# Kernel tuning notes

Hardware: AMD Instinct MI355X
Metric: run time of the kernel (lower is better)

The kernel has to match this reference:

```python
import jax, jax.numpy as jnp
import numpy as np

ALPHA = 2.0      # spikingjelly surrogate.ATan default alpha
TAU_LIF = 2.0    # LIFNode tau
V_TH = 1.0       # spike threshold (v_reset = 0.0, hard reset)


@jax.custom_vjp
def spike_fn(x):
    # Heaviside forward (spikingjelly: x >= 0 -> 1)
    return (x >= 0.0).astype(x.dtype)

def _spike_fwd(x):
    return spike_fn(x), x

def _spike_bwd(x, g):
    # ATan surrogate gradient: alpha/2 / (1 + (pi/2 * alpha * x)^2)
    return (g * (ALPHA / 2.0) / (1.0 + (jnp.pi / 2.0 * ALPHA * x) ** 2),)

spike_fn.defvjp(_spike_fwd, _spike_bwd)


def setup_inputs() -> dict:
    key = jax.random.key(0)
    ks = jax.random.split(key, 5)
    B, T, I, H, O = 256, 1000, 700, 64, 20
    x = jax.random.normal(ks[0], (B, T, I), dtype=jnp.float32)
    W_h = jax.random.normal(ks[1], (H, I), dtype=jnp.float32) / np.sqrt(I).astype(np.float32)
    b_h = jnp.zeros((H,), dtype=jnp.float32)
    W_r = jax.random.normal(ks[2], (O, H), dtype=jnp.float32) / np.sqrt(H).astype(np.float32)
    b_r = jnp.zeros((O,), dtype=jnp.float32)
    tau_m = jax.random.uniform(ks[3], (O,), dtype=jnp.float32, minval=0.0, maxval=4.0)
    return {"x": x, "W_h": W_h, "b_h": b_h, "W_r": W_r, "b_r": b_r, "tau_m": tau_m}


def reference(x, W_h, b_h, W_r, b_r, tau_m):
    B, T, I = x.shape
    H = W_h.shape[0]
    O = W_r.shape[0]
    # One big GEMM for all hidden input currents: [T, B, H]
    currents = jnp.einsum('bti,hi->tbh', x, W_h) + b_h
    beta = jax.nn.sigmoid(tau_m)  # readout leak [O]
    # original accumulates softmax only for t > 10
    mask = (jnp.arange(T) > 10).astype(x.dtype)

    def step(carry, inp):
        v, v_ro, acc = carry
        cur, m = inp
        # LIF charge (decay_input=True, v_reset=0): v += (cur - v)/tau
        v = v + (cur - v) / TAU_LIF
        s = spike_fn(v - V_TH)
        # hard reset to v_reset = 0
        v = v * (1.0 - s)
        # readout leaky integrator
        ro_in = s @ W_r.T + b_r                      # [B, O]
        v_ro = v_ro * beta + (1.0 - beta) * ro_in
        acc = acc + m * jax.nn.softmax(v_ro, axis=-1)
        return (v, v_ro, acc), None

    init = (jnp.zeros((B, H), x.dtype),
            jnp.zeros((B, O), x.dtype),
            jnp.zeros((B, O), x.dtype))
    (_, _, acc), _ = jax.lax.scan(step, init, (currents, mask))
    return acc
```

## Files before the change

### kernel.cpp

```cpp
#include <hip/hip_runtime.h>


typedef float  f32x4  __attribute__((ext_vector_type(4)));
typedef short  short8 __attribute__((ext_vector_type(8)));
typedef unsigned long long ull;

#define B_   256
#define T_   1000
#define K_   700
#define H_   64
#define O_   20
#define NKT  11
#define NCH  200
#define TCH  5
#define TCL  100
#define NCL  10
#define BIL  40

#define OFF_WFRAG  ((size_t)0)
#define OFF_CUR    ((size_t)262144)
#define OFF_MASK   ((size_t)65798144)

__global__ void wprep(const float* __restrict__ Wh, unsigned short* __restrict__ wfrag) {
    int e = blockIdx.x * 256 + threadIdx.x;
    int kt   = e >> 9;
    int rem  = e & 511;
    int nf   = rem >> 7;
    int kf   = (rem >> 6) & 1;
    int lane = rem & 63;
    int h     = nf * 16 + (lane & 15);
    int kbase = kt * 64 + kf * 32 + ((lane >> 4) & 3) * 8;
    int slot  = (nf * 2 + kf) * 64 + lane;
    unsigned short* dh = wfrag + (size_t)kt * 8192 + slot * 8;
    unsigned short* dl = dh + 4096;
#pragma unroll
    for (int j = 0; j < 8; ++j) {
        int k = kbase + j;
        float v = (k < K_) ? Wh[(size_t)h * K_ + k] : 0.0f;
        unsigned u  = __builtin_bit_cast(unsigned, v);
        float    fh = __builtin_bit_cast(float, u & 0xffff0000u);
        float    r  = v - fh;
        dh[j] = (unsigned short)(u >> 16);
        dl[j] = (unsigned short)(__builtin_bit_cast(unsigned, r) >> 16);
    }
}

__device__ __forceinline__ void glds16(const void* src, void* lds) {
    __builtin_amdgcn_global_load_lds(
        (const __attribute__((address_space(1))) void*)src,
        (__attribute__((address_space(3))) void*)lds, 16, 0, 0);
}

__device__ __forceinline__ void splitpair(f32x4 p0, f32x4 p1, short8& hi, short8& lo) {
#pragma unroll
    for (int j = 0; j < 4; ++j) {
        {
            unsigned u  = __builtin_bit_cast(unsigned, p0[j]);
            float    fh = __builtin_bit_cast(float, u & 0xffff0000u);
            float    r  = p0[j] - fh;
            hi[j] = (short)(u >> 16);
            lo[j] = (short)(__builtin_bit_cast(unsigned, r) >> 16);
        }
        {
            unsigned u  = __builtin_bit_cast(unsigned, p1[j]);
            float    fh = __builtin_bit_cast(float, u & 0xffff0000u);
            float    r  = p1[j] - fh;
            hi[j + 4] = (short)(u >> 16);
            lo[j + 4] = (short)(__builtin_bit_cast(unsigned, r) >> 16);
        }
    }
}

__device__ __forceinline__ void stage_x64(const float* __restrict__ x, size_t row0,
                                          int kt, int tid, float* sbuf) {
#pragma unroll
    for (int j = 0; j < 4; ++j) {
        int id = j * 256 + tid;
        int s  = id >> 9;
        int r  = (id >> 3) & 63;
        int pc = id & 7;
        int c  = pc ^ (r & 7);
        int kbyte = kt * 256 + s * 128 + (c << 4);
        if (kbyte + 16 > K_ * 4) kbyte = 0;
        const char* src = (const char*)(x + (row0 + r) * (size_t)K_) + kbyte;
        float* dst = sbuf + (size_t)(id & ~63) * 4;
        glds16(src, dst);
    }
}

__device__ __forceinline__ void stage_w64(const unsigned short* __restrict__ wfrag,
                                          int kt, int tid, unsigned short* sbuf) {
#pragma unroll
    for (int j = 0; j < 4; ++j) {
        int id = j * 256 + tid;
        const unsigned short* src = wfrag + (size_t)kt * 8192 + id * 8;
        unsigned short* dst = sbuf + (size_t)(id & ~63) * 8;
        glds16(src, dst);
    }
}

__device__ __forceinline__ void compute64(const float* sbx_, const unsigned short* sbw_,
                                          int lane, int wid, f32x4 (&acc)[4]) {
    const char*   xb = (const char*)sbx_;
    const short8* wb = (const short8*)sbw_;
    int rloc = wid * 16 + (lane & 15);
    int g2   = ((lane >> 4) & 3) * 2;
#pragma unroll
    for (int kf = 0; kf < 2; ++kf) {
        const char* base = xb + kf * 8192 + rloc * 128;
        int c0 = g2 ^ (rloc & 7);
        int c1 = (g2 + 1) ^ (rloc & 7);
        f32x4 p0 = *(const f32x4*)(base + c0 * 16);
        f32x4 p1 = *(const f32x4*)(base + c1 * 16);
        short8 ah, al;
        splitpair(p0, p1, ah, al);
#pragma unroll
        for (int n = 0; n < 4; ++n) {
            short8 bhf = wb[(n * 2 + kf) * 64 + lane];
            short8 blf = wb[(n * 2 + kf) * 64 + lane + 512];
            acc[n] = __builtin_amdgcn_mfma_f32_16x16x32_bf16(ah, bhf, acc[n], 0, 0, 0);
            acc[n] = __builtin_amdgcn_mfma_f32_16x16x32_bf16(al, bhf, acc[n], 0, 0, 0);
            acc[n] = __builtin_amdgcn_mfma_f32_16x16x32_bf16(ah, blf, acc[n], 0, 0, 0);
        }
    }
}

__global__ __launch_bounds__(256, 2) void gemm_cur(const float* __restrict__ x,
                                                   const unsigned short* __restrict__ wfrag,
                                                   const float* __restrict__ b_h,
                                                   float* __restrict__ cur) {
    __shared__ float          sbx[2][4096];
    __shared__ unsigned short sbw[2][8192];
    int tid  = threadIdx.x;
    int lane = tid & 63;
    int wid  = tid >> 6;
    size_t row0 = (size_t)blockIdx.x * 64;

    float bh4[4];
#pragma unroll
    for (int n = 0; n < 4; ++n) bh4[n] = b_h[n * 16 + (lane & 15)];

    f32x4 acc[4];
#pragma unroll
    for (int n = 0; n < 4; ++n) acc[n] = (f32x4){0.f, 0.f, 0.f, 0.f};

    stage_x64(x, row0, 0, tid, sbx[0]);  stage_w64(wfrag, 0, tid, sbw[0]);
    stage_x64(x, row0, 1, tid, sbx[1]);  stage_w64(wfrag, 1, tid, sbw[1]);

#define GSTEP(T, N)                                                          \
    {                                                                        \
        asm volatile("s_waitcnt vmcnt(" #N ")" ::: "memory");                \
        __builtin_amdgcn_s_barrier();                                        \
        compute64(sbx[(T) & 1], sbw[(T) & 1], lane, wid, acc);               \
        asm volatile("s_waitcnt lgkmcnt(0)" ::: "memory");                   \
        __builtin_amdgcn_s_barrier();                                        \
        if ((T) + 2 < NKT) {                                                 \
            stage_x64(x, row0, (T) + 2, tid, sbx[(T) & 1]);                  \
            stage_w64(wfrag, (T) + 2, tid, sbw[(T) & 1]);                    \
        }                                                                    \
    }
    GSTEP(0, 8)   GSTEP(1, 8)   GSTEP(2, 8)   GSTEP(3, 8)   GSTEP(4, 8)
    GSTEP(5, 8)   GSTEP(6, 8)   GSTEP(7, 8)   GSTEP(8, 8)   GSTEP(9, 8)
    GSTEP(10, 0)
#undef GSTEP

    f32x4* cur4 = (f32x4*)cur;
    size_t r4 = row0 + wid * 16 + ((lane >> 4) & 3) * 4;
#pragma unroll
    for (int n = 0; n < 4; ++n) {
        f32x4 q;
#pragma unroll
        for (int j = 0; j < 4; ++j) q[j] = acc[n][j] + bh4[n];
        cur4[(r4 >> 2) * 64 + n * 16 + (lane & 15)] = q;
    }
}

__global__ __launch_bounds__(64) void lif(const float* __restrict__ cur, ull* __restrict__ masks) {
    int b = blockIdx.x & 255;
    int c = blockIdx.x >> 8;
    int h = threadIdx.x;
    int t0 = c * TCL;
    int ts = (c == 0) ? 0 : (t0 - BIL);
    const f32x4* p = (const f32x4*)cur + (((size_t)b * T_ + ts) >> 2) * 64 + h;
    float v = 0.0f;
    int ngb = (t0 - ts) >> 2;
    for (int g = 0; g < ngb; ++g) {
        f32x4 q = p[g * 64];
#pragma unroll
        for (int j = 0; j < 4; ++j) {
            v = (v + q[j]) * 0.5f;
            v = (v >= 1.0f) ? 0.0f : v;
        }
    }
    p += (size_t)ngb * 64;
    ull* mp = masks + (size_t)b * T_ + t0;
#pragma unroll 2
    for (int g = 0; g < TCL / 4; ++g) {
        f32x4 q = p[g * 64];
#pragma unroll
        for (int j = 0; j < 4; ++j) {
            v = (v + q[j]) * 0.5f;
            bool s = (v >= 1.0f);
            ull m = __ballot(s);
            if (h == 0) mp[g * 4 + j] = m;
            v = s ? 0.0f : v;
        }
    }
}

__global__ __launch_bounds__(512) void readout(const ull* __restrict__ masks,
                                               const float* __restrict__ Wr,
                                               const float* __restrict__ br,
                                               const float* __restrict__ tau,
                                               float* __restrict__ out) {
    __shared__ __align__(16) float wt[64][20];
    __shared__ ull  smask[T_];
    __shared__ __align__(16) float E[NCH][20];
    __shared__ __align__(16) float Sv[NCH][20];
    __shared__ __align__(16) float pacc[NCH][20];
    __shared__ __align__(16) float sScale[20], sBase[20], sBeta[20];
    __shared__ float Pg[8][20], Sst[8][20], part[8][20];

    int tid = threadIdx.x;
    int b   = blockIdx.x;
    for (int i = tid; i < 1280; i += 512) wt[i & 63][i >> 6] = Wr[(size_t)(i >> 6) * 64 + (i & 63)];
    for (int i = tid; i < T_; i += 512) smask[i] = masks[(size_t)b * T_ + i];
    if (tid < 20) {
        float beta = 1.0f / (1.0f + __expf(-tau[tid]));
        sBeta[tid]  = beta;
        sScale[tid] = 1.0f - beta;
        sBase[tid]  = br[tid];
    }
    __syncthreads();

    for (int it = tid; it < NCH * 5; it += 512) {
        int o4 = it % 5;
        int c  = it / 5;
        f32x4 beta4  = *(const f32x4*)&sBeta[o4 * 4];
        f32x4 scale4 = *(const f32x4*)&sScale[o4 * 4];
        f32x4 base4  = *(const f32x4*)&sBase[o4 * 4];
        f32x4 v = {0.f, 0.f, 0.f, 0.f};
        const ull* mp = smask + c * TCH;
#pragma unroll
        for (int j = 0; j < TCH; ++j) {
            ull m = mp[j];
            f32x4 a = {0.f, 0.f, 0.f, 0.f};
            while (m) {
                int h = __builtin_ctzll(m);
                m &= (m - 1);
                a += *(const f32x4*)&wt[h][o4 * 4];
            }
            f32x4 q;
#pragma unroll
            for (int jj = 0; jj < 4; ++jj) q[jj] = scale4[jj] * (base4[jj] + a[jj]);
            v = beta4 * v + q;
        }
        *(f32x4*)&E[c][o4 * 4] = v;
    }
    __syncthreads();

    if (tid < 160) {
        int o = tid >> 3, g = tid & 7;
        float beta = sBeta[o];
        float b2 = beta * beta;
        float bp = b2 * b2 * beta;
        float P = 0.0f;
        for (int c = g * 25; c < g * 25 + 25; ++c) P = bp * P + E[c][o];
        Pg[g][o] = P;
    }
    __syncthreads();

    if (tid < 20) {
        int o = tid;
        float beta = sBeta[o];
        float b2 = beta * beta;
        float bp = b2 * b2 * beta;
        float bp25 = 1.0f;
#pragma unroll
        for (int i = 0; i < 25; ++i) bp25 *= bp;
        float s = 0.0f;
        for (int g = 0; g < 8; ++g) { Sst[g][o] = s; s = bp25 * s + Pg[g][o]; }
    }
    __syncthreads();

    if (tid < 160) {
        int o = tid >> 3, g = tid & 7;
        float beta = sBeta[o];
        float b2 = beta * beta;
        float bp = b2 * b2 * beta;
        float s = Sst[g][o];
        for (int c = g * 25; c < g * 25 + 25; ++c) { Sv[c][o] = s; s = bp * s + E[c][o]; }
    }
    __syncthreads();

    if (tid < NCH) {
        int c = tid;
        float beta[20], v[20], acc[20];
#pragma unroll
        for (int o = 0; o < 20; ++o) {
            beta[o] = sBeta[o];
            v[o]   = Sv[c][o];
            acc[o] = 0.0f;
        }
        int t0 = c * TCH;
        const ull* mp = smask + t0;
#pragma unroll
        for (int j = 0; j < TCH; ++j) {
            int t = t0 + j;
            ull m = mp[j];
            f32x4 a[5];
#pragma unroll
            for (int i = 0; i < 5; ++i) a[i] = (f32x4){0.f, 0.f, 0.f, 0.f};
            while (m) {
                int h = __builtin_ctzll(m);
                m &= (m - 1);
                const f32x4* w4 = (const f32x4*)&wt[h][0];
#pragma unroll
                for (int i = 0; i < 5; ++i) a[i] += w4[i];
            }
#pragma unroll
            for (int o = 0; o < 20; ++o) {
                float q = sScale[o] * (sBase[o] + a[o >> 2][o & 3]);
                v[o] = beta[o] * v[o] + q;
            }
            if (t >= 11) {
                float mx = v[0];
#pragma unroll
                for (int o = 1; o < 20; ++o) mx = fmaxf(mx, v[o]);
                float e[20], ssum = 0.0f;
#pragma unroll
                for (int o = 0; o < 20; ++o) { e[o] = __expf(v[o] - mx); ssum += e[o]; }
                float inv = 1.0f / ssum;
#pragma unroll
                for (int o = 0; o < 20; ++o) acc[o] += e[o] * inv;
            }
        }
#pragma unroll
        for (int o = 0; o < 20; ++o) pacc[c][o] = acc[o];
    }
    __syncthreads();

    if (tid < 160) {
        int o = tid >> 3, g = tid & 7;
        float s = 0.0f;
        for (int c = g * 25; c < g * 25 + 25; ++c) s += pacc[c][o];
        part[g][o] = s;
    }
    __syncthreads();
    if (tid < 20) {
        float s = 0.0f;
#pragma unroll
        for (int g = 0; g < 8; ++g) s += part[g][tid];
        out[(size_t)b * 20 + tid] = s;
    }
}

extern "C" void kernel_launch(void* const* d_in, const int* in_sizes, int n_in,
                              void* d_out, int out_size, void* d_ws, size_t ws_size,
                              hipStream_t stream) {
    const float* x   = (const float*)d_in[0];
    const float* W_h = (const float*)d_in[1];
    const float* b_h = (const float*)d_in[2];
    const float* W_r = (const float*)d_in[3];
    const float* b_r = (const float*)d_in[4];
    const float* tau = (const float*)d_in[5];

    char* ws = (char*)d_ws;
    unsigned short* wfrag = (unsigned short*)(ws + OFF_WFRAG);
    float* cur  = (float*)(ws + OFF_CUR);
    ull*   msk  = (ull*)(ws + OFF_MASK);
    float* out  = (float*)d_out;

    wprep<<<22, 256, 0, stream>>>(W_h, wfrag);
    gemm_cur<<<4000, 256, 0, stream>>>(x, wfrag, b_h, cur);
    lif<<<NCL * 256, 64, 0, stream>>>(cur, msk);
    readout<<<256, 512, 0, stream>>>(msk, W_r, b_r, tau, out);
}
```

Baseline: 222.1 us.

## Fuse GEMM, LIF scan and readout into one per-batch kernel

Replaces the separate current-GEMM, LIF and readout kernels with a single kernel that runs one 512-thread block per batch element. Each block streams its own x rows in 128-timestep tiles, writes the input currents for a tile into shared memory, runs the LIF recurrence there to build spike masks, then runs the existing readout in reused shared memory. This avoids the global round trip of the large current tensor and two kernel launches. In exchange, the grid shrinks to 256 large blocks with heavy LDS use, likely one block per CU. The serial LIF phase between tiles also stalls the GEMM load pipeline, which may hurt memory-bandwidth utilisation.

```diff
diff --git a/kernel.cpp b/kernel.cpp
--- a/kernel.cpp
+++ b/kernel.cpp
@@ -11,15 +11,11 @@
 #define H_   64
 #define O_   20
 #define NKT  11
+#define NMT  8
 #define NCH  200
 #define TCH  5
-#define TCL  100
-#define NCL  10
-#define BIL  40
 
 #define OFF_WFRAG  ((size_t)0)
-#define OFF_CUR    ((size_t)262144)
-#define OFF_MASK   ((size_t)65798144)
 
 __global__ void wprep(const float* __restrict__ Wh, unsigned short* __restrict__ wfrag) {
     int e = blockIdx.x * 256 + threadIdx.x;
@@ -71,43 +67,45 @@
     }
 }
 
-__device__ __forceinline__ void stage_x64(const float* __restrict__ x, size_t row0,
-                                          int kt, int tid, float* sbuf) {
+__device__ __forceinline__ void stage_x(const float* __restrict__ x, size_t brow0,
+                                        int mt, int kt, int tid, float* sbuf) {
 #pragma unroll
     for (int j = 0; j < 4; ++j) {
-        int id = j * 256 + tid;
-        int s  = id >> 9;
-        int r  = (id >> 3) & 63;
+        int id = j * 512 + tid;
+        int s2 = id >> 10;
+        int r  = (id >> 3) & 127;
         int pc = id & 7;
         int c  = pc ^ (r & 7);
-        int kbyte = kt * 256 + s * 128 + (c << 4);
+        int trow = mt * 128 + r;
+        if (trow >= T_) trow = 0;
+        int kbyte = kt * 256 + s2 * 128 + (c << 4);
         if (kbyte + 16 > K_ * 4) kbyte = 0;
-        const char* src = (const char*)(x + (row0 + r) * (size_t)K_) + kbyte;
+        const char* src = (const char*)(x + (brow0 + trow) * (size_t)K_) + kbyte;
         float* dst = sbuf + (size_t)(id & ~63) * 4;
         glds16(src, dst);
     }
 }
 
-__device__ __forceinline__ void stage_w64(const unsigned short* __restrict__ wfrag,
-                                          int kt, int tid, unsigned short* sbuf) {
-#pragma unroll
-    for (int j = 0; j < 4; ++j) {
-        int id = j * 256 + tid;
+__device__ __forceinline__ void stage_w(const unsigned short* __restrict__ wfrag,
+                                        int kt, int tid, unsigned short* sbuf) {
+#pragma unroll
+    for (int j = 0; j < 2; ++j) {
+        int id = j * 512 + tid;
         const unsigned short* src = wfrag + (size_t)kt * 8192 + id * 8;
         unsigned short* dst = sbuf + (size_t)(id & ~63) * 8;
         glds16(src, dst);
     }
 }
 
-__device__ __forceinline__ void compute64(const float* sbx_, const unsigned short* sbw_,
-                                          int lane, int wid, f32x4 (&acc)[4]) {
+__device__ __forceinline__ void compute128(const float* sbx_, const unsigned short* sbw_,
+                                           int lane, int wid, f32x4 (&acc)[4]) {
     const char*   xb = (const char*)sbx_;
     const short8* wb = (const short8*)sbw_;
     int rloc = wid * 16 + (lane & 15);
     int g2   = ((lane >> 4) & 3) * 2;
 #pragma unroll
     for (int kf = 0; kf < 2; ++kf) {
-        const char* base = xb + kf * 8192 + rloc * 128;
+        const char* base = xb + kf * 16384 + rloc * 128;
         int c0 = g2 ^ (rloc & 7);
         int c1 = (g2 + 1) ^ (rloc & 7);
         f32x4 p0 = *(const f32x4*)(base + c0 * 16);
@@ -125,16 +123,27 @@
     }
 }
 
-__global__ __launch_bounds__(256, 2) void gemm_cur(const float* __restrict__ x,
-                                                   const unsigned short* __restrict__ wfrag,
-                                                   const float* __restrict__ b_h,
-                                                   float* __restrict__ cur) {
-    __shared__ float          sbx[2][4096];
-    __shared__ unsigned short sbw[2][8192];
+__global__ __launch_bounds__(512, 2) void fused(const float* __restrict__ x,
+                                                const unsigned short* __restrict__ wfrag,
+                                                const float* __restrict__ b_h,
+                                                const float* __restrict__ Wr,
+                                                const float* __restrict__ br,
+                                                const float* __restrict__ tau,
+                                                float* __restrict__ out) {
+    __shared__ __align__(16) char  pool[98304];
+    __shared__ __align__(16) float curT[128 * 64];
+    __shared__ ull smaskL[T_];
+
     int tid  = threadIdx.x;
     int lane = tid & 63;
     int wid  = tid >> 6;
-    size_t row0 = (size_t)blockIdx.x * 64;
+    int b    = blockIdx.x;
+    size_t brow0 = (size_t)b * T_;
+
+    float*          sbx0 = (float*)pool;
+    float*          sbx1 = (float*)(pool + 32768);
+    unsigned short* sbw0 = (unsigned short*)(pool + 65536);
+    unsigned short* sbw1 = (unsigned short*)(pool + 81920);
 
     float bh4[4];
 #pragma unroll
@@ -143,88 +152,71 @@
     f32x4 acc[4];
 #pragma unroll
     for (int n = 0; n < 4; ++n) acc[n] = (f32x4){0.f, 0.f, 0.f, 0.f};
-
-    stage_x64(x, row0, 0, tid, sbx[0]);  stage_w64(wfrag, 0, tid, sbw[0]);
-    stage_x64(x, row0, 1, tid, sbx[1]);  stage_w64(wfrag, 1, tid, sbw[1]);
-
-#define GSTEP(T, N)                                                          \
-    {                                                                        \
-        asm volatile("s_waitcnt vmcnt(" #N ")" ::: "memory");                \
-        __builtin_amdgcn_s_barrier();                                        \
-        compute64(sbx[(T) & 1], sbw[(T) & 1], lane, wid, acc);               \
-        asm volatile("s_waitcnt lgkmcnt(0)" ::: "memory");                   \
-        __builtin_amdgcn_s_barrier();                                        \
-        if ((T) + 2 < NKT) {                                                 \
-            stage_x64(x, row0, (T) + 2, tid, sbx[(T) & 1]);                  \
-            stage_w64(wfrag, (T) + 2, tid, sbw[(T) & 1]);                    \
-        }                                                                    \
-    }
-    GSTEP(0, 8)   GSTEP(1, 8)   GSTEP(2, 8)   GSTEP(3, 8)   GSTEP(4, 8)
-    GSTEP(5, 8)   GSTEP(6, 8)   GSTEP(7, 8)   GSTEP(8, 8)   GSTEP(9, 8)
-    GSTEP(10, 0)
-#undef GSTEP
-
-    f32x4* cur4 = (f32x4*)cur;
-    size_t r4 = row0 + wid * 16 + ((lane >> 4) & 3) * 4;
-#pragma unroll
-    for (int n = 0; n < 4; ++n) {
-        f32x4 q;
-#pragma unroll
-        for (int j = 0; j < 4; ++j) q[j] = acc[n][j] + bh4[n];
-        cur4[(r4 >> 2) * 64 + n * 16 + (lane & 15)] = q;
-    }
-}
-
-__global__ __launch_bounds__(64) void lif(const float* __restrict__ cur, ull* __restrict__ masks) {
-    int b = blockIdx.x & 255;
-    int c = blockIdx.x >> 8;
-    int h = threadIdx.x;
-    int t0 = c * TCL;
-    int ts = (c == 0) ? 0 : (t0 - BIL);
-    const f32x4* p = (const f32x4*)cur + (((size_t)b * T_ + ts) >> 2) * 64 + h;
     float v = 0.0f;
-    int ngb = (t0 - ts) >> 2;
-    for (int g = 0; g < ngb; ++g) {
-        f32x4 q = p[g * 64];
-#pragma unroll
-        for (int j = 0; j < 4; ++j) {
-            v = (v + q[j]) * 0.5f;
-            v = (v >= 1.0f) ? 0.0f : v;
-        }
-    }
-    p += (size_t)ngb * 64;
-    ull* mp = masks + (size_t)b * T_ + t0;
-#pragma unroll 2
-    for (int g = 0; g < TCL / 4; ++g) {
-        f32x4 q = p[g * 64];
-#pragma unroll
-        for (int j = 0; j < 4; ++j) {
-            v = (v + q[j]) * 0.5f;
-            bool s = (v >= 1.0f);
-            ull m = __ballot(s);
-            if (h == 0) mp[g * 4 + j] = m;
-            v = s ? 0.0f : v;
-        }
-    }
-}
-
-__global__ __launch_bounds__(512) void readout(const ull* __restrict__ masks,
-                                               const float* __restrict__ Wr,
-                                               const float* __restrict__ br,
-                                               const float* __restrict__ tau,
-                                               float* __restrict__ out) {
-    __shared__ __align__(16) float wt[64][20];
-    __shared__ ull  smask[T_];
-    __shared__ __align__(16) float E[NCH][20];
-    __shared__ __align__(16) float Sv[NCH][20];
-    __shared__ __align__(16) float pacc[NCH][20];
-    __shared__ __align__(16) float sScale[20], sBase[20], sBeta[20];
-    __shared__ float Pg[8][20], Sst[8][20], part[8][20];
-
-    int tid = threadIdx.x;
-    int b   = blockIdx.x;
-    for (int i = tid; i < 1280; i += 512) wt[i & 63][i >> 6] = Wr[(size_t)(i >> 6) * 64 + (i & 63)];
-    for (int i = tid; i < T_; i += 512) smask[i] = masks[(size_t)b * T_ + i];
+
+    stage_x(x, brow0, 0, 0, tid, sbx0);  stage_w(wfrag, 0, tid, sbw0);
+    stage_x(x, brow0, 0, 1, tid, sbx1);  stage_w(wfrag, 1, tid, sbw1);
+
+    int p = 0;
+    for (int mt = 0; mt < NMT; ++mt) {
+#pragma unroll
+        for (int kt = 0; kt <= 10; ++kt) {
+            float*          xb = p ? sbx1 : sbx0;
+            unsigned short* wb = p ? sbw1 : sbw0;
+            if (kt == 10 && mt == NMT - 1) {
+                asm volatile("s_waitcnt vmcnt(0)" ::: "memory");
+            } else {
+                asm volatile("s_waitcnt vmcnt(6)" ::: "memory");
+            }
+            __builtin_amdgcn_s_barrier();
+            compute128(xb, wb, lane, wid, acc);
+            if (kt == 10) {
+#pragma unroll
+                for (int n = 0; n < 4; ++n) {
+#pragma unroll
+                    for (int j = 0; j < 4; ++j) {
+                        int tloc = wid * 16 + ((lane >> 4) & 3) * 4 + j;
+                        curT[tloc * 64 + n * 16 + (lane & 15)] = acc[n][j] + bh4[n];
+                    }
+                    acc[n] = (f32x4){0.f, 0.f, 0.f, 0.f};
+                }
+            }
+            asm volatile("s_waitcnt lgkmcnt(0)" ::: "memory");
+            __builtin_amdgcn_s_barrier();
+            int smt = mt, skt = kt + 2;
+            if (skt >= NKT) { smt += 1; skt -= NKT; }
+            if (smt < NMT) {
+                stage_x(x, brow0, smt, skt, tid, xb);
+                stage_w(wfrag, skt, tid, wb);
+            }
+            p ^= 1;
+            if (kt == 10) {
+                int tcnt = T_ - mt * 128; if (tcnt > 128) tcnt = 128;
+                for (int j = 0; j < tcnt; ++j) {
+                    float c = curT[j * 64 + lane];
+                    v = (v + c) * 0.5f;
+                    bool sp = (v >= 1.0f);
+                    ull m = __ballot(sp);
+                    if (wid == (j >> 4) && lane == 0) smaskL[mt * 128 + j] = m;
+                    v = sp ? 0.0f : v;
+                }
+            }
+        }
+    }
+    __syncthreads();
+
+    float* wt     = (float*)pool;
+    float (*E)[20]    = (float(*)[20])(pool + 5120);
+    float (*Sv)[20]   = (float(*)[20])(pool + 21120);
+    float (*pacc)[20] = (float(*)[20])(pool + 37120);
+    float* sScale = (float*)(pool + 53120);
+    float* sBase  = (float*)(pool + 53216);
+    float* sBeta  = (float*)(pool + 53312);
+    float (*Pg)[20]   = (float(*)[20])(pool + 53408);
+    float (*Sst)[20]  = (float(*)[20])(pool + 54048);
+    float (*part)[20] = (float(*)[20])(pool + 54688);
+
+    for (int i = tid; i < 1280; i += 512) wt[(i & 63) * 20 + (i >> 6)] = Wr[(size_t)(i >> 6) * 64 + (i & 63)];
     if (tid < 20) {
         float beta = 1.0f / (1.0f + __expf(-tau[tid]));
         sBeta[tid]  = beta;
@@ -239,8 +231,8 @@
         f32x4 beta4  = *(const f32x4*)&sBeta[o4 * 4];
         f32x4 scale4 = *(const f32x4*)&sScale[o4 * 4];
         f32x4 base4  = *(const f32x4*)&sBase[o4 * 4];
-        f32x4 v = {0.f, 0.f, 0.f, 0.f};
-        const ull* mp = smask + c * TCH;
+        f32x4 vv = {0.f, 0.f, 0.f, 0.f};
+        const ull* mp = smaskL + c * TCH;
 #pragma unroll
         for (int j = 0; j < TCH; ++j) {
             ull m = mp[j];
@@ -248,14 +240,14 @@
             while (m) {
                 int h = __builtin_ctzll(m);
                 m &= (m - 1);
-                a += *(const f32x4*)&wt[h][o4 * 4];
+                a += *(const f32x4*)&wt[h * 20 + o4 * 4];
             }
             f32x4 q;
 #pragma unroll
             for (int jj = 0; jj < 4; ++jj) q[jj] = scale4[jj] * (base4[jj] + a[jj]);
-            v = beta4 * v + q;
-        }
-        *(f32x4*)&E[c][o4 * 4] = v;
+            vv = beta4 * vv + q;
+        }
+        *(f32x4*)&E[c][o4 * 4] = vv;
     }
     __syncthreads();
 
@@ -295,15 +287,15 @@
 
     if (tid < NCH) {
         int c = tid;
-        float beta[20], v[20], acc[20];
+        float beta[20], vv[20], ac[20];
 #pragma unroll
         for (int o = 0; o < 20; ++o) {
             beta[o] = sBeta[o];
-            v[o]   = Sv[c][o];
-            acc[o] = 0.0f;
+            vv[o]  = Sv[c][o];
+            ac[o]  = 0.0f;
         }
         int t0 = c * TCH;
-        const ull* mp = smask + t0;
+        const ull* mp = smaskL + t0;
 #pragma unroll
         for (int j = 0; j < TCH; ++j) {
             int t = t0 + j;
@@ -314,29 +306,29 @@
             while (m) {
                 int h = __builtin_ctzll(m);
                 m &= (m - 1);
-                const f32x4* w4 = (const f32x4*)&wt[h][0];
+                const f32x4* w4 = (const f32x4*)&wt[h * 20];
 #pragma unroll
                 for (int i = 0; i < 5; ++i) a[i] += w4[i];
             }
 #pragma unroll
             for (int o = 0; o < 20; ++o) {
                 float q = sScale[o] * (sBase[o] + a[o >> 2][o & 3]);
-                v[o] = beta[o] * v[o] + q;
+                vv[o] = beta[o] * vv[o] + q;
             }
             if (t >= 11) {
-                float mx = v[0];
-#pragma unroll
-                for (int o = 1; o < 20; ++o) mx = fmaxf(mx, v[o]);
+                float mx = vv[0];
+#pragma unroll
+                for (int o = 1; o < 20; ++o) mx = fmaxf(mx, vv[o]);
                 float e[20], ssum = 0.0f;
 #pragma unroll
-                for (int o = 0; o < 20; ++o) { e[o] = __expf(v[o] - mx); ssum += e[o]; }
+                for (int o = 0; o < 20; ++o) { e[o] = __expf(vv[o] - mx); ssum += e[o]; }
                 float inv = 1.0f / ssum;
 #pragma unroll
-                for (int o = 0; o < 20; ++o) acc[o] += e[o] * inv;
-            }
-        }
-#pragma unroll
-        for (int o = 0; o < 20; ++o) pacc[c][o] = acc[o];
+                for (int o = 0; o < 20; ++o) ac[o] += e[o] * inv;
+            }
+        }
+#pragma unroll
+        for (int o = 0; o < 20; ++o) pacc[c][o] = ac[o];
     }
     __syncthreads();
 
@@ -367,12 +359,8 @@
 
     char* ws = (char*)d_ws;
     unsigned short* wfrag = (unsigned short*)(ws + OFF_WFRAG);
-    float* cur  = (float*)(ws + OFF_CUR);
-    ull*   msk  = (ull*)(ws + OFF_MASK);
-    float* out  = (float*)d_out;
+    float* out = (float*)d_out;
 
     wprep<<<22, 256, 0, stream>>>(W_h, wfrag);
-    gemm_cur<<<4000, 256, 0, stream>>>(x, wfrag, b_h, cur);
-    lif<<<NCL * 256, 64, 0, stream>>>(cur, msk);
-    readout<<<256, 512, 0, stream>>>(msk, W_r, b_r, tau, out);
-}
+    fused<<<B_, 512, 0, stream>>>(x, wfrag, b_h, W_r, b_r, tau, out);
+}
```

After: 219.9 us. About the same (-1.0%).
